# Optimization experiments

Measured on AMD Instinct MI355X. Metric: run time of the kernel, lower is better.

## Reference

```python
import jax, jax.numpy as jnp
import numpy as np

EPS = 1e-12  # torch F.normalize clamp

N, C, H, W = 32, 128, 128, 128
K = 64  # num_clusters


def setup_inputs() -> dict:
    key = jax.random.key(0)
    k1, k2, k3 = jax.random.split(key, 3)
    x = jax.random.normal(k1, (N, C, H, W), dtype=jnp.float32)
    conv_w = jax.random.normal(k2, (K, C), dtype=jnp.float32) * 0.1  # 1x1 conv weight, no bias
    centroids = jax.random.uniform(k3, (K, C), dtype=jnp.float32)   # torch.rand init
    return {"x": x, "conv_w": conv_w, "centroids": centroids}


def reference(x, conv_w, centroids):
    n, c = x.shape[:2]
    xf = x.reshape(n, c, -1)                       # [N, C, S], S = H*W
    # 1x1 conv == per-location matmul over channels
    soft_assign = jnp.einsum('kc,ncs->nks', conv_w, xf)
    soft_assign = jax.nn.softmax(soft_assign, axis=1)   # softmax over clusters
    # vlad[n,k,c] = sum_s a[n,k,s] * (x[n,c,s] - centroid[k,c])
    #            = (a @ x^T) - (sum_s a) * centroid   (avoids per-cluster residual tensors)
    vlad = jnp.einsum('nks,ncs->nkc', soft_assign, xf) \
           - soft_assign.sum(axis=-1)[..., None] * centroids[None, :, :]
    # intra-normalization over descriptor dim
    vlad = vlad / jnp.maximum(jnp.linalg.norm(vlad, axis=2, keepdims=True), EPS)
    flat = vlad.reshape(n, -1)                     # [N, K*C]
    flat = flat / jnp.maximum(jnp.linalg.norm(flat, axis=1, keepdims=True), EPS)
    return flat
```

## Files before the change

kernel.cpp:

```cpp
#include <hip/hip_runtime.h>

#define N_ 32
#define C_ 128
#define K_ 64
#define S_ 16384
#define TS 64
#define NBPN 24
#define NTILES (S_/TS)
#define NBLK (N_*NBPN)
#define XS 136
#define WS 136
#define PS 72
#define EPS 1e-12f

typedef __attribute__((ext_vector_type(8))) _Float16 half8;
typedef __attribute__((ext_vector_type(4))) _Float16 half4;
typedef __attribute__((ext_vector_type(4))) float floatx4;

__device__ __forceinline__ int swz(int row, int c) {
  return (((c >> 4) ^ (row & 7)) << 4) | (c & 15);
}

#define BAR_LDS()                                            \
  do {                                                       \
    __builtin_amdgcn_sched_barrier(0);                       \
    asm volatile("s_waitcnt lgkmcnt(0)" ::: "memory");       \
    __builtin_amdgcn_s_barrier();                            \
    __builtin_amdgcn_sched_barrier(0);                       \
  } while (0)

template <bool SLAB>
__global__ __launch_bounds__(256, 4) void vlad_main(
    const float* __restrict__ x, const float* __restrict__ w,
    float* __restrict__ vlad_out, float* __restrict__ asum_out) {
  __shared__ _Float16 sXT[TS * XS];
  __shared__ _Float16 sW[K_ * WS];
  __shared__ _Float16 sP[K_ * PS];
  __shared__ float sRed[4 * K_];

  const int tid = threadIdx.x;
  const int lane = tid & 63;
  const int wv = tid >> 6;
  const int lm = lane & 15;
  const int quad = lane >> 4;

  const int bid = blockIdx.x;
  const int n = bid / NBPN;
  const int j = bid % NBPN;
  const int ts = (j * NTILES) / NBPN;
  const int te = ((j + 1) * NTILES) / NBPN;

  for (int idx = tid; idx < K_ * C_; idx += 256) {
    int kc = idx >> 7, c = idx & 127;
    sW[kc * WS + swz(kc, c)] = (_Float16)w[idx];
  }

  floatx4 acc[2][4];
#pragma unroll
  for (int i = 0; i < 2; ++i)
#pragma unroll
    for (int k = 0; k < 4; ++k) acc[i][k] = (floatx4){0.f, 0.f, 0.f, 0.f};
  float accA[4] = {0.f, 0.f, 0.f, 0.f};

  const int cw = tid & 15;
  const int sq = tid >> 4;
  const float* xn = x + (size_t)n * C_ * S_;

  float4 pf[8];
  {
    const float* p = xn + (size_t)(8 * cw) * S_ + ts * TS + 4 * sq;
#pragma unroll
    for (int r = 0; r < 8; ++r) pf[r] = *(const float4*)(p + (size_t)r * S_);
  }

  __syncthreads();

  for (int t = ts; t < te; ++t) {
    const int s0 = t * TS;

    float4 gxa[2][2], gxb[2][2];
#pragma unroll
    for (int ci = 0; ci < 2; ++ci) {
      const float* p = xn + (size_t)((2 * wv + ci) * 16 + lm) * S_ + s0 + quad * 8;
      gxa[ci][0] = *(const float4*)p;
      gxa[ci][1] = *(const float4*)(p + 4);
      gxb[ci][0] = *(const float4*)(p + 32);
      gxb[ci][1] = *(const float4*)(p + 36);
    }

#pragma unroll
    for (int u = 0; u < 4; ++u) {
      const int s = 4 * sq + u;
      half8 hv;
#pragma unroll
      for (int r = 0; r < 8; ++r) {
        float f = (u == 0) ? pf[r].x : (u == 1) ? pf[r].y : (u == 2) ? pf[r].z : pf[r].w;
        hv[r] = (_Float16)f;
      }
      *(half8*)&sXT[s * XS + swz(s, 8 * cw)] = hv;
    }
    BAR_LDS();

    floatx4 D[4];
#pragma unroll
    for (int k = 0; k < 4; ++k) D[k] = (floatx4){0.f, 0.f, 0.f, 0.f};
    const int srow = wv * 16 + lm;
#pragma unroll
    for (int ks = 0; ks < 4; ++ks) {
      half8 Af = *(const half8*)&sXT[srow * XS + swz(srow, ks * 32 + quad * 8)];
#pragma unroll
      for (int kt = 0; kt < 4; ++kt) {
        const int krow = kt * 16 + lm;
        half8 Wf = *(const half8*)&sW[krow * WS + swz(krow, ks * 32 + quad * 8)];
        D[kt] = __builtin_amdgcn_mfma_f32_16x16x32_f16(Af, Wf, D[kt], 0, 0, 0);
      }
    }

#pragma unroll
    for (int r = 0; r < 4; ++r) {
      float e0 = __expf(D[0][r]), e1 = __expf(D[1][r]),
            e2 = __expf(D[2][r]), e3 = __expf(D[3][r]);
      float sum = e0 + e1 + e2 + e3;
      sum += __shfl_xor(sum, 1);
      sum += __shfl_xor(sum, 2);
      sum += __shfl_xor(sum, 4);
      sum += __shfl_xor(sum, 8);
      float inv = 1.f / sum;
      D[0][r] = e0 * inv; D[1][r] = e1 * inv;
      D[2][r] = e2 * inv; D[3][r] = e3 * inv;
    }
#pragma unroll
    for (int kt = 0; kt < 4; ++kt) {
      accA[kt] += D[kt][0] + D[kt][1] + D[kt][2] + D[kt][3];
      half4 hp = {(_Float16)D[kt][0], (_Float16)D[kt][1],
                  (_Float16)D[kt][2], (_Float16)D[kt][3]};
      *(half4*)&sP[(kt * 16 + lm) * PS + wv * 16 + quad * 4] = hp;
    }

    if (t + 1 < te) {
      const float* p = xn + (size_t)(8 * cw) * S_ + (t + 1) * TS + 4 * sq;
#pragma unroll
      for (int r = 0; r < 8; ++r) pf[r] = *(const float4*)(p + (size_t)r * S_);
    }
    BAR_LDS();

    {
      half8 Bp[4];
#pragma unroll
      for (int kt = 0; kt < 4; ++kt)
        Bp[kt] = *(const half8*)&sP[(kt * 16 + lm) * PS + quad * 8];
#pragma unroll
      for (int ci = 0; ci < 2; ++ci) {
        half8 Ax = {(_Float16)gxa[ci][0].x, (_Float16)gxa[ci][0].y,
                    (_Float16)gxa[ci][0].z, (_Float16)gxa[ci][0].w,
                    (_Float16)gxa[ci][1].x, (_Float16)gxa[ci][1].y,
                    (_Float16)gxa[ci][1].z, (_Float16)gxa[ci][1].w};
#pragma unroll
        for (int kt = 0; kt < 4; ++kt)
          acc[ci][kt] = __builtin_amdgcn_mfma_f32_16x16x32_f16(Ax, Bp[kt], acc[ci][kt], 0, 0, 0);
      }
    }
    {
      half8 Bp[4];
#pragma unroll
      for (int kt = 0; kt < 4; ++kt)
        Bp[kt] = *(const half8*)&sP[(kt * 16 + lm) * PS + 32 + quad * 8];
#pragma unroll
      for (int ci = 0; ci < 2; ++ci) {
        half8 Ax = {(_Float16)gxb[ci][0].x, (_Float16)gxb[ci][0].y,
                    (_Float16)gxb[ci][0].z, (_Float16)gxb[ci][0].w,
                    (_Float16)gxb[ci][1].x, (_Float16)gxb[ci][1].y,
                    (_Float16)gxb[ci][1].z, (_Float16)gxb[ci][1].w};
#pragma unroll
        for (int kt = 0; kt < 4; ++kt)
          acc[ci][kt] = __builtin_amdgcn_mfma_f32_16x16x32_f16(Ax, Bp[kt], acc[ci][kt], 0, 0, 0);
      }
    }
  }

  float* vb = vlad_out + (SLAB ? (size_t)bid : (size_t)n) * (K_ * C_);
#pragma unroll
  for (int ci = 0; ci < 2; ++ci) {
    const int c0 = (2 * wv + ci) * 16 + quad * 4;
#pragma unroll
    for (int kt = 0; kt < 4; ++kt) {
      const int kc = kt * 16 + lm;
      if (SLAB) {
        *(floatx4*)(vb + kc * C_ + c0) = acc[ci][kt];
      } else {
#pragma unroll
        for (int r = 0; r < 4; ++r)
          atomicAdd(vb + kc * C_ + c0 + r, acc[ci][kt][r]);
      }
    }
  }

#pragma unroll
  for (int kt = 0; kt < 4; ++kt) {
    float v = accA[kt];
    v += __shfl_xor(v, 16);
    v += __shfl_xor(v, 32);
    if (quad == 0) sRed[wv * K_ + kt * 16 + lm] = v;
  }
  __syncthreads();
  if (tid < K_) {
    float s = sRed[tid] + sRed[K_ + tid] + sRed[2 * K_ + tid] + sRed[3 * K_ + tid];
    if (SLAB) asum_out[(size_t)bid * K_ + tid] = s;
    else atomicAdd(asum_out + n * K_ + tid, s);
  }
}

template <bool SLAB>
__global__ __launch_bounds__(128) void vlad_intra(
    const float* __restrict__ vlad_in, const float* __restrict__ asum_in,
    const float* __restrict__ cent, float* __restrict__ vlad_norm,
    float* __restrict__ gnorm) {
  const int bid = blockIdx.x;
  const int n = bid >> 6, k = bid & 63;
  const int c = threadIdx.x;

  float v, a;
  if (SLAB) {
    v = 0.f; a = 0.f;
#pragma unroll 4
    for (int ch = 0; ch < NBPN; ++ch) {
      v += vlad_in[((size_t)(n * NBPN + ch) * K_ + k) * C_ + c];
      a += asum_in[(n * NBPN + ch) * K_ + k];
    }
  } else {
    v = vlad_in[((size_t)(n * K_ + k)) * C_ + c];
    a = asum_in[n * K_ + k];
  }
  v -= a * cent[k * C_ + c];

  float ss = v * v;
  ss += __shfl_xor(ss, 1);  ss += __shfl_xor(ss, 2);  ss += __shfl_xor(ss, 4);
  ss += __shfl_xor(ss, 8);  ss += __shfl_xor(ss, 16); ss += __shfl_xor(ss, 32);
  __shared__ float red[2];
  if ((threadIdx.x & 63) == 0) red[threadIdx.x >> 6] = ss;
  __syncthreads();
  float total = red[0] + red[1];
  float nrm = fmaxf(sqrtf(total), EPS);
  vlad_norm[((size_t)(n * K_ + k)) * C_ + c] = v / nrm;
  if (threadIdx.x == 0) atomicAdd(gnorm + n, total / (nrm * nrm));
}

__global__ __launch_bounds__(256) void vlad_final(
    const float* __restrict__ vlad_norm, const float* __restrict__ gnorm,
    float* __restrict__ out) {
  const int idx = blockIdx.x * 256 + threadIdx.x;
  if (idx >= N_ * K_ * C_) return;
  float g = gnorm[idx >> 13];
  out[idx] = vlad_norm[idx] / fmaxf(sqrtf(g), EPS);
}

extern "C" void kernel_launch(void* const* d_in, const int* in_sizes, int n_in,
                              void* d_out, int out_size, void* d_ws, size_t ws_size,
                              hipStream_t stream) {
  const float* x    = (const float*)d_in[0];
  const float* w    = (const float*)d_in[1];
  const float* cent = (const float*)d_in[2];
  float* out = (float*)d_out;

  const size_t slab_f = (size_t)NBLK * K_ * C_;
  const size_t asum_f = (size_t)NBLK * K_;
  const size_t norm_f = (size_t)N_ * K_ * C_;
  const size_t need = (slab_f + asum_f + norm_f + N_) * sizeof(float);

  if (ws_size >= need) {
    float* slab  = (float*)d_ws;
    float* asums = slab + slab_f;
    float* vnorm = asums + asum_f;
    float* gnorm = vnorm + norm_f;
    hipMemsetAsync(gnorm, 0, N_ * sizeof(float), stream);
    vlad_main<true><<<dim3(NBLK), dim3(256), 0, stream>>>(x, w, slab, asums);
    vlad_intra<true><<<dim3(N_ * K_), dim3(128), 0, stream>>>(slab, asums, cent, vnorm, gnorm);
    vlad_final<<<dim3((N_ * K_ * C_ + 255) / 256), dim3(256), 0, stream>>>(vnorm, gnorm, out);
  } else {
    float* vlad_acc = (float*)d_ws;
    float* asum_g   = vlad_acc + norm_f;
    float* gnorm    = asum_g + N_ * K_;
    hipMemsetAsync(d_ws, 0, (norm_f + N_ * K_ + N_) * sizeof(float), stream);
    vlad_main<false><<<dim3(NBLK), dim3(256), 0, stream>>>(x, w, vlad_acc, asum_g);
    vlad_intra<false><<<dim3(N_ * K_), dim3(128), 0, stream>>>(vlad_acc, asum_g, cent, vlad_acc, gnorm);
    vlad_final<<<dim3((N_ * K_ * C_ + 255) / 256), dim3(256), 0, stream>>>(vlad_acc, gnorm, out);
  }
}
```

Measured before the change: 413.5 us.

## Load x once per tile and reuse registers for LDS transpose and second GEMM

Before, each tile of x was read from global memory twice: once through a transposed prefetch into LDS for the logits GEMM and once as row fragments for the aggregation GEMM. Now each thread loads its row fragments once, converts them to half, writes them into LDS with scalar transposed stores using a new XOR swizzle, and reuses the same half registers as the B operand of the aggregation MFMA with swapped operand order. This halves global traffic for x but adds scalar 16-bit LDS stores that may cause bank conflicts, and the output writes become scalar rather than vector stores.

```diff
diff --git a/kernel.cpp b/kernel.cpp
--- a/kernel.cpp
+++ b/kernel.cpp
@@ -62,42 +62,58 @@
     for (int k = 0; k < 4; ++k) acc[i][k] = (floatx4){0.f, 0.f, 0.f, 0.f};
   float accA[4] = {0.f, 0.f, 0.f, 0.f};
 
-  const int cw = tid & 15;
-  const int sq = tid >> 4;
   const float* xn = x + (size_t)n * C_ * S_;
-
-  float4 pf[8];
-  {
-    const float* p = xn + (size_t)(8 * cw) * S_ + ts * TS + 4 * sq;
-#pragma unroll
-    for (int r = 0; r < 8; ++r) pf[r] = *(const float4*)(p + (size_t)r * S_);
-  }
+  const float* xrow[2];
+  xrow[0] = xn + (size_t)((2 * wv + 0) * 16 + lm) * S_;
+  xrow[1] = xn + (size_t)((2 * wv + 1) * 16 + lm) * S_;
+
+  float4 gx[2][2][2];
+#pragma unroll
+  for (int ci = 0; ci < 2; ++ci)
+#pragma unroll
+    for (int sl = 0; sl < 2; ++sl) {
+      const float* p = xrow[ci] + ts * TS + sl * 32 + quad * 8;
+      gx[ci][sl][0] = *(const float4*)p;
+      gx[ci][sl][1] = *(const float4*)(p + 4);
+    }
 
   __syncthreads();
 
   for (int t = ts; t < te; ++t) {
-    const int s0 = t * TS;
-
-    float4 gxa[2][2], gxb[2][2];
+    half8 hx[2][2];
+#pragma unroll
+    for (int ci = 0; ci < 2; ++ci)
+#pragma unroll
+      for (int sl = 0; sl < 2; ++sl) {
+        half8 h;
+        h[0] = (_Float16)gx[ci][sl][0].x; h[1] = (_Float16)gx[ci][sl][0].y;
+        h[2] = (_Float16)gx[ci][sl][0].z; h[3] = (_Float16)gx[ci][sl][0].w;
+        h[4] = (_Float16)gx[ci][sl][1].x; h[5] = (_Float16)gx[ci][sl][1].y;
+        h[6] = (_Float16)gx[ci][sl][1].z; h[7] = (_Float16)gx[ci][sl][1].w;
+        hx[ci][sl] = h;
+      }
 #pragma unroll
     for (int ci = 0; ci < 2; ++ci) {
-      const float* p = xn + (size_t)((2 * wv + ci) * 16 + lm) * S_ + s0 + quad * 8;
-      gxa[ci][0] = *(const float4*)p;
-      gxa[ci][1] = *(const float4*)(p + 4);
-      gxb[ci][0] = *(const float4*)(p + 32);
-      gxb[ci][1] = *(const float4*)(p + 36);
-    }
-
-#pragma unroll
-    for (int u = 0; u < 4; ++u) {
-      const int s = 4 * sq + u;
-      half8 hv;
-#pragma unroll
-      for (int r = 0; r < 8; ++r) {
-        float f = (u == 0) ? pf[r].x : (u == 1) ? pf[r].y : (u == 2) ? pf[r].z : pf[r].w;
-        hv[r] = (_Float16)f;
-      }
-      *(half8*)&sXT[s * XS + swz(s, 8 * cw)] = hv;
+#pragma unroll
+      for (int sl = 0; sl < 2; ++sl) {
+        const int key = sl * 4 + quad;
+        const int blk = (2 * wv + ci) ^ key;
+        const int base = (sl * 32 + quad * 8) * XS + blk * 16 + lm;
+#pragma unroll
+        for (int jj = 0; jj < 8; ++jj)
+          sXT[base + jj * XS] = hx[ci][sl][jj];
+      }
+    }
+
+    if (t + 1 < te) {
+#pragma unroll
+      for (int ci = 0; ci < 2; ++ci)
+#pragma unroll
+        for (int sl = 0; sl < 2; ++sl) {
+          const float* p = xrow[ci] + (t + 1) * TS + sl * 32 + quad * 8;
+          gx[ci][sl][0] = *(const float4*)p;
+          gx[ci][sl][1] = *(const float4*)(p + 4);
+        }
     }
     BAR_LDS();
 
@@ -105,9 +121,12 @@
 #pragma unroll
     for (int k = 0; k < 4; ++k) D[k] = (floatx4){0.f, 0.f, 0.f, 0.f};
     const int srow = wv * 16 + lm;
+    const int rkey = (srow >> 3) & 7;
 #pragma unroll
     for (int ks = 0; ks < 4; ++ks) {
-      half8 Af = *(const half8*)&sXT[srow * XS + swz(srow, ks * 32 + quad * 8)];
+      const int cb = ks * 32 + quad * 8;
+      const int blk = (cb >> 4) ^ rkey;
+      half8 Af = *(const half8*)&sXT[srow * XS + blk * 16 + (cb & 15)];
 #pragma unroll
       for (int kt = 0; kt < 4; ++kt) {
         const int krow = kt * 16 + lm;
@@ -136,61 +155,37 @@
                   (_Float16)D[kt][2], (_Float16)D[kt][3]};
       *(half4*)&sP[(kt * 16 + lm) * PS + wv * 16 + quad * 4] = hp;
     }
-
-    if (t + 1 < te) {
-      const float* p = xn + (size_t)(8 * cw) * S_ + (t + 1) * TS + 4 * sq;
-#pragma unroll
-      for (int r = 0; r < 8; ++r) pf[r] = *(const float4*)(p + (size_t)r * S_);
-    }
     BAR_LDS();
 
-    {
-      half8 Bp[4];
+#pragma unroll
+    for (int sl = 0; sl < 2; ++sl) {
+      half8 Pf[4];
 #pragma unroll
       for (int kt = 0; kt < 4; ++kt)
-        Bp[kt] = *(const half8*)&sP[(kt * 16 + lm) * PS + quad * 8];
-#pragma unroll
-      for (int ci = 0; ci < 2; ++ci) {
-        half8 Ax = {(_Float16)gxa[ci][0].x, (_Float16)gxa[ci][0].y,
-                    (_Float16)gxa[ci][0].z, (_Float16)gxa[ci][0].w,
-                    (_Float16)gxa[ci][1].x, (_Float16)gxa[ci][1].y,
-                    (_Float16)gxa[ci][1].z, (_Float16)gxa[ci][1].w};
+        Pf[kt] = *(const half8*)&sP[(kt * 16 + lm) * PS + sl * 32 + quad * 8];
+#pragma unroll
+      for (int ci = 0; ci < 2; ++ci)
 #pragma unroll
         for (int kt = 0; kt < 4; ++kt)
-          acc[ci][kt] = __builtin_amdgcn_mfma_f32_16x16x32_f16(Ax, Bp[kt], acc[ci][kt], 0, 0, 0);
-      }
-    }
-    {
-      half8 Bp[4];
-#pragma unroll
-      for (int kt = 0; kt < 4; ++kt)
-        Bp[kt] = *(const half8*)&sP[(kt * 16 + lm) * PS + 32 + quad * 8];
-#pragma unroll
-      for (int ci = 0; ci < 2; ++ci) {
-        half8 Ax = {(_Float16)gxb[ci][0].x, (_Float16)gxb[ci][0].y,
-                    (_Float16)gxb[ci][0].z, (_Float16)gxb[ci][0].w,
-                    (_Float16)gxb[ci][1].x, (_Float16)gxb[ci][1].y,
-                    (_Float16)gxb[ci][1].z, (_Float16)gxb[ci][1].w};
-#pragma unroll
-        for (int kt = 0; kt < 4; ++kt)
-          acc[ci][kt] = __builtin_amdgcn_mfma_f32_16x16x32_f16(Ax, Bp[kt], acc[ci][kt], 0, 0, 0);
-      }
+          acc[ci][kt] = __builtin_amdgcn_mfma_f32_16x16x32_f16(
+              Pf[kt], hx[ci][sl], acc[ci][kt], 0, 0, 0);
     }
   }
 
   float* vb = vlad_out + (SLAB ? (size_t)bid : (size_t)n) * (K_ * C_);
 #pragma unroll
   for (int ci = 0; ci < 2; ++ci) {
-    const int c0 = (2 * wv + ci) * 16 + quad * 4;
+    const int c = (2 * wv + ci) * 16 + lm;
 #pragma unroll
     for (int kt = 0; kt < 4; ++kt) {
-      const int kc = kt * 16 + lm;
-      if (SLAB) {
-        *(floatx4*)(vb + kc * C_ + c0) = acc[ci][kt];
-      } else {
-#pragma unroll
-        for (int r = 0; r < 4; ++r)
-          atomicAdd(vb + kc * C_ + c0 + r, acc[ci][kt][r]);
+      const int kc0 = kt * 16 + quad * 4;
+#pragma unroll
+      for (int r = 0; r < 4; ++r) {
+        if (SLAB) {
+          vb[(size_t)(kc0 + r) * C_ + c] = acc[ci][kt][r];
+        } else {
+          atomicAdd(vb + (size_t)(kc0 + r) * C_ + c, acc[ci][kt][r]);
+        }
       }
     }
   }
```

After: 398.0 us. 3.7% less time.
